# Performance work log

Hardware: AMD Instinct MI355X
Metric: run time of the kernel (lower is better)

The kernel has to match this reference:

```python
import jax, jax.numpy as jnp
import numpy as np

NEG_RATIO = 5          # neg_sample_ratio, also k (num_nodes-1 >> ratio)
THRESH = 0.7           # hard_neg_threshold
SMOOTH = 0.1           # label_smoothing
NUM_NODES = 200_000
DIM = 128
B = 1024               # batch size, all labels == 1 (all positives)
FILL_VAL = -1.0e9


def _l2_normalize(x, eps=1e-12):
    # F.normalize(p=2, dim=-1): divide by clamped L2 norm
    n = jnp.sqrt(jnp.sum(x * x, axis=-1, keepdims=True))
    return x / jnp.maximum(n, eps)


def setup_inputs() -> dict:
    key = jax.random.key(0)
    k1, k2, k3, k4 = jax.random.split(key, 4)
    src_nodes = jax.random.randint(k1, (B,), 0, NUM_NODES)
    dst_nodes = jax.random.randint(k2, (B,), 0, NUM_NODES)
    labels = jnp.ones((B,), dtype=jnp.float32)  # all positives -> pos_mask all True
    timestamps = jax.random.uniform(k3, (B,), dtype=jnp.float32)
    memory = jax.random.normal(k4, (NUM_NODES, DIM), dtype=jnp.float32)
    return {
        "src_nodes": src_nodes,
        "dst_nodes": dst_nodes,
        "labels": labels,
        "timestamps": timestamps,
        "memory": memory,
    }


def reference(src_nodes, dst_nodes, labels, timestamps, memory):
    # --- embedding gather + L2 normalize ---
    src_emb = memory[src_nodes]                      # [B, D]
    s = _l2_normalize(src_emb).astype(jnp.float16)   # use_half_precision=True
    c = _l2_normalize(memory).astype(jnp.float16)    # [N, D]

    # --- similarity [B, N], back to fp32 ---
    sim = jnp.matmul(s, c.T).astype(jnp.float32)

    # --- mask out ground-truth dst and below-threshold sims ---
    cols = jnp.arange(NUM_NODES)
    allowed = cols[None, :] != dst_nodes[:, None]    # exclude GT positives
    valid = allowed & (sim > THRESH)
    score = jnp.where(valid, sim, FILL_VAL)

    # --- top-k hard negatives per positive ---
    k = NEG_RATIO  # min(neg_sample_ratio, num_nodes-1)
    topk_vals, topk_idx = jax.lax.top_k(score, k)    # [B, k]
    is_real = (topk_vals > FILL_VAL + 1.0).reshape(-1)  # [B*k]

    # --- fallback random negatives (fixed-shape equivalent of the torch
    #     pack-real-then-pad-random assembly; total count == B*k either way) ---
    rkey = jax.random.key(42)
    rand_dst = jax.random.randint(rkey, (B * k,), 0, NUM_NODES)
    src_rep = jnp.repeat(src_nodes, k)               # [B*k]
    rand_dst = jnp.where(rand_dst == src_rep, (rand_dst + 1) % NUM_NODES, rand_dst)

    final_src = src_rep
    final_dst = jnp.where(is_real, topk_idx.reshape(-1), rand_dst)
    neg_ts = jnp.repeat(timestamps, k)

    # --- assemble augmented batch ---
    new_src = jnp.concatenate([src_nodes, final_src])
    new_dst = jnp.concatenate([dst_nodes, final_dst])
    new_labels = jnp.concatenate([labels, jnp.zeros((B * k,), labels.dtype)])
    new_ts = jnp.concatenate([timestamps, neg_ts])

    # --- label smoothing ---
    new_labels = new_labels * (1.0 - SMOOTH) + (1.0 - new_labels) * SMOOTH

    return new_src, new_dst, new_labels, new_ts, topk_vals
```

## Files before the change

kernel.cpp:

```cpp
#include <hip/hip_runtime.h>

#define NUM_NODES 200000
#define DIM 128
#define BATCH 1024
#define K_NEG 5
#define CAP 16
#define NBLK 250
#define CPB 800
#define TCOL 32
#define NT 25
#define THRESH 0.7f
#define FILL (-1.0e9f)

typedef __attribute__((ext_vector_type(8))) short short8;
typedef __attribute__((ext_vector_type(16))) float f32x16;

__device__ __forceinline__ unsigned short f2bf(float x) {
  unsigned u = __builtin_bit_cast(unsigned, x);
  return (unsigned short)((u + 0x7fffu + ((u >> 16) & 1u)) >> 16);
}

__device__ __forceinline__ void stage16(const void* g, void* l) {
  __builtin_amdgcn_global_load_lds(
      (const __attribute__((address_space(1))) unsigned int*)g,
      (__attribute__((address_space(3))) unsigned int*)l,
      16, 0, 0);
}

__device__ __forceinline__ void tf2x32(unsigned k0, unsigned k1,
                                       unsigned x0, unsigned x1,
                                       unsigned* o0, unsigned* o1) {
  unsigned ks2 = k0 ^ k1 ^ 0x1BD11BDAu;
  unsigned v0 = x0 + k0, v1 = x1 + k1;
#define TFR(r) { v0 += v1; v1 = (v1 << r) | (v1 >> (32 - r)); v1 ^= v0; }
  TFR(13) TFR(15) TFR(26) TFR(6)   v0 += k1;  v1 += ks2 + 1u;
  TFR(17) TFR(29) TFR(16) TFR(24)  v0 += ks2; v1 += k0 + 2u;
  TFR(13) TFR(15) TFR(26) TFR(6)   v0 += k0;  v1 += k1 + 3u;
  TFR(17) TFR(29) TFR(16) TFR(24)  v0 += k1;  v1 += ks2 + 4u;
  TFR(13) TFR(15) TFR(26) TFR(6)   v0 += ks2; v1 += k0 + 5u;
#undef TFR
  *o0 = v0; *o1 = v1;
}

__device__ __forceinline__ unsigned rbits32(unsigned ka, unsigned kb, unsigned m) {
  unsigned o0, o1;
  tf2x32(ka, kb, 0u, m, &o0, &o1);
  return o0 ^ o1;
}

__global__ void prep_kernel(const float* __restrict__ memory,
                            const int* __restrict__ src_nodes,
                            unsigned short* __restrict__ s16f,
                            int* __restrict__ cand_cnt) {
  int tid = threadIdx.x;
  int gid = blockIdx.x * 256 + tid;
  if (gid < BATCH) cand_cnt[gid] = 0;
  int row = blockIdx.x * 4 + (tid >> 6);
  int L = tid & 63;
  int s = src_nodes[row];
  float2 v = ((const float2*)(memory + (size_t)s * DIM))[L];
  float ss = v.x * v.x + v.y * v.y;
#pragma unroll
  for (int off = 32; off > 0; off >>= 1) ss += __shfl_xor(ss, off);
  float inv = 1.0f / fmaxf(sqrtf(ss), 1e-12f);
  unsigned p = (unsigned)f2bf(v.x * inv) | ((unsigned)f2bf(v.y * inv) << 16);
  int ms = row >> 5, l32 = row & 31;
  int c = L >> 2;
  int ks = c >> 1, half = c & 1;
  ((unsigned*)s16f)[(((ms * 8 + ks) * 64) + half * 32 + l32) * 4 + (L & 3)] = p;
}

__global__ __launch_bounds__(512, 2) void sim_scan_kernel(
    const float* __restrict__ memory,
    const unsigned short* __restrict__ s16f,
    const int* __restrict__ dst_nodes,
    int* __restrict__ cand_cnt,
    float* __restrict__ cand_val,
    int* __restrict__ cand_idx) {
  __shared__ char rawb[16384];
  __shared__ unsigned short fragb[2][4096];
  __shared__ float nrmb[2][32];

  int tid = threadIdx.x;
  int wid = tid >> 6;
  int lane = tid & 63;
  int half = lane >> 5;
  int l32 = lane & 31;
  int jb0 = blockIdx.x * CPB;

  const char* mb = (const char*)memory;

#define STAGE(t) {                                                              \
    int jn = jb0 + (t) * TCOL;                                                  \
    stage16(mb + (size_t)(jn + (tid & 31)) * 512 + ((tid >> 5) << 4),           \
            (char*)rawb + (wid << 10));                                         \
    stage16(mb + (size_t)(jn + (tid & 31)) * 512 + (((tid >> 5) + 16) << 4),    \
            (char*)rawb + 8192 + (wid << 10));                                  \
  }

  int ccol = wid * 4 + (lane & 3);
  int cseg = lane >> 2;
#define CONVERT(p) {                                                            \
    float4 q0 = *(const float4*)(rawb + (((2 * cseg) * 32 + ccol) << 4));       \
    float4 q1 = *(const float4*)(rawb + (((2 * cseg + 1) * 32 + ccol) << 4));   \
    float ss = q0.x * q0.x + q0.y * q0.y + q0.z * q0.z + q0.w * q0.w            \
             + q1.x * q1.x + q1.y * q1.y + q1.z * q1.z + q1.w * q1.w;           \
    ss += __shfl_xor(ss, 4); ss += __shfl_xor(ss, 8);                           \
    ss += __shfl_xor(ss, 16); ss += __shfl_xor(ss, 32);                         \
    short8 f;                                                                   \
    f[0] = (short)f2bf(q0.x); f[1] = (short)f2bf(q0.y);                         \
    f[2] = (short)f2bf(q0.z); f[3] = (short)f2bf(q0.w);                         \
    f[4] = (short)f2bf(q1.x); f[5] = (short)f2bf(q1.y);                         \
    f[6] = (short)f2bf(q1.z); f[7] = (short)f2bf(q1.w);                         \
    *(short8*)((char*)fragb[p] + ((cseg * 32 + ccol) << 4)) = f;                \
    if (cseg == 0) nrmb[p][ccol] = fmaxf(sqrtf(ss), 1e-12f);                    \
  }

  STAGE(0);
  const short8* __restrict__ af = (const short8*)s16f;
  short8 a[4][8];
#pragma unroll
  for (int m = 0; m < 4; ++m)
#pragma unroll
    for (int ks = 0; ks < 8; ++ks)
      a[m][ks] = af[(((wid * 4 + m) * 8) + ks) * 64 + lane];
  __syncthreads();
  CONVERT(0);
  __syncthreads();
  STAGE(1);
  __syncthreads();

  f32x16 Z;
#pragma unroll
  for (int i = 0; i < 16; ++i) Z[i] = 0.0f;

  for (int t = 0; t < NT; ++t) {
    if (t < NT - 1) CONVERT((t + 1) & 1);
    __syncthreads();
    if (t < NT - 2) STAGE(t + 2);

    int p = t & 1;
    float nv = nrmb[p][l32];
    float thr = THRESH * nv;
    float invv = 1.0f / nv;
    int gj = jb0 + t * TCOL + l32;
    short8 bf[8];
#pragma unroll
    for (int ks = 0; ks < 8; ++ks)
      bf[ks] = *(const short8*)((char*)fragb[p] + (((2 * ks + half) * 32 + l32) << 4));

#pragma unroll
    for (int mp = 0; mp < 2; ++mp) {
      f32x16 accA = __builtin_amdgcn_mfma_f32_32x32x16_bf16(a[mp * 2][0], bf[0], Z, 0, 0, 0);
      f32x16 accB = __builtin_amdgcn_mfma_f32_32x32x16_bf16(a[mp * 2 + 1][0], bf[0], Z, 0, 0, 0);
#pragma unroll
      for (int ks = 1; ks < 8; ++ks) {
        accA = __builtin_amdgcn_mfma_f32_32x32x16_bf16(a[mp * 2][ks], bf[ks], accA, 0, 0, 0);
        accB = __builtin_amdgcn_mfma_f32_32x32x16_bf16(a[mp * 2 + 1][ks], bf[ks], accB, 0, 0, 0);
      }
      float mA = accA[0], mB = accB[0];
#pragma unroll
      for (int i = 1; i < 16; ++i) { mA = fmaxf(mA, accA[i]); mB = fmaxf(mB, accB[i]); }
      if (mA > thr || mB > thr) {
#pragma unroll
        for (int e = 0; e < 2; ++e) {
#pragma unroll
          for (int r = 0; r < 16; ++r) {
            float raw = (e == 0) ? accA[r] : accB[r];
            if (raw > thr) {
              int gi = (wid * 4 + mp * 2 + e) * 32 + (r & 3) + 8 * (r >> 2) + 4 * half;
              if (gj != dst_nodes[gi]) {
                int pq = atomicAdd(&cand_cnt[gi], 1);
                if (pq < CAP) {
                  cand_val[gi * CAP + pq] = raw * invv;
                  cand_idx[gi * CAP + pq] = gj;
                }
              }
            }
          }
        }
      }
    }

    __syncthreads();
  }
#undef STAGE
#undef CONVERT
}

__global__ void finalize_kernel(const int* __restrict__ src_nodes,
                                const int* __restrict__ dst_nodes,
                                const float* __restrict__ labels,
                                const float* __restrict__ ts,
                                const int* __restrict__ cand_cnt,
                                const float* __restrict__ cand_val,
                                const int* __restrict__ cand_idx,
                                float* __restrict__ out) {
  int r = blockIdx.x * 256 + threadIdx.x;
  if (r >= BATCH) return;
  const int TOT = BATCH + BATCH * K_NEG;
  int srcv = src_nodes[r];
  float tsv = ts[r];
  out[r] = (float)srcv;
  out[TOT + r] = (float)dst_nodes[r];
  float l = labels[r];
  out[2 * TOT + r] = l * 0.9f + (1.0f - l) * 0.1f;
  out[3 * TOT + r] = tsv;

  int cnt = cand_cnt[r];
  cnt = cnt < CAP ? cnt : CAP;
  float cv[CAP]; int ci[CAP];
  for (int i = 0; i < cnt; ++i) { cv[i] = cand_val[r * CAP + i]; ci[i] = cand_idx[r * CAP + i]; }

  unsigned k1a, k1b, k2a, k2b;
  tf2x32(0u, 42u, 0u, 0u, &k1a, &k1b);
  tf2x32(0u, 42u, 0u, 1u, &k2a, &k2b);

  const unsigned span = 200000u;
  const unsigned mult = 167296u;

  for (int s = 0; s < K_NEG; ++s) {
    int sel = -1;
    for (int i = 0; i < cnt; ++i)
      if (sel < 0 || cv[i] > cv[sel] || (cv[i] == cv[sel] && ci[i] < ci[sel])) sel = i;
    float v = FILL; int idx = 0;
    if (sel >= 0) { v = cv[sel]; idx = ci[sel]; cv[sel] = FILL; ci[sel] = 0x7fffffff; }
    bool is_real = v > (FILL + 1.0f);

    unsigned m = (unsigned)(r * K_NEG + s);
    unsigned hi = rbits32(k1a, k1b, m);
    unsigned lo = rbits32(k2a, k2b, m);
    unsigned off = ((hi % span) * mult + (lo % span)) % span;
    int rd = (int)off;
    if (rd == srcv) rd = (rd + 1) % NUM_NODES;
    int fd = is_real ? idx : rd;

    int mi = (int)m;
    out[BATCH + mi] = (float)srcv;
    out[TOT + BATCH + mi] = (float)fd;
    out[2 * TOT + BATCH + mi] = 0.1f;
    out[3 * TOT + BATCH + mi] = tsv;
    out[4 * TOT + mi] = v;
  }
}

extern "C" void kernel_launch(void* const* d_in, const int* in_sizes, int n_in,
                              void* d_out, int out_size, void* d_ws, size_t ws_size,
                              hipStream_t stream) {
  const int* src = (const int*)d_in[0];
  const int* dst = (const int*)d_in[1];
  const float* labels = (const float*)d_in[2];
  const float* ts = (const float*)d_in[3];
  const float* memory = (const float*)d_in[4];
  float* out = (float*)d_out;

  char* ws = (char*)d_ws;
  unsigned short* s16f = (unsigned short*)ws;
  int* cand_cnt = (int*)(ws + 262144);
  float* cand_val = (float*)(ws + 266240);
  int* cand_idx = (int*)(ws + 331776);

  prep_kernel<<<256, 256, 0, stream>>>(memory, src, s16f, cand_cnt);
  sim_scan_kernel<<<NBLK, 512, 0, stream>>>(memory, s16f, dst, cand_cnt, cand_val, cand_idx);
  finalize_kernel<<<(BATCH + 255) / 256, 256, 0, stream>>>(src, dst, labels, ts,
                                                           cand_cnt, cand_val, cand_idx, out);
}
```

Before: 188.5 us.

## Double-buffer raw LDS staging with XOR swizzle and drop a barrier

```diff
diff --git a/kernel.cpp b/kernel.cpp
--- a/kernel.cpp
+++ b/kernel.cpp
@@ -77,7 +77,7 @@
     int* __restrict__ cand_cnt,
     float* __restrict__ cand_val,
     int* __restrict__ cand_idx) {
-  __shared__ char rawb[16384];
+  __shared__ char rawb[2][16384];
   __shared__ unsigned short fragb[2][4096];
   __shared__ float nrmb[2][32];
 
@@ -90,19 +90,25 @@
 
   const char* mb = (const char*)memory;
 
-#define STAGE(t) {                                                              \
+#define STAGE(t, rbuf) {                                                        \
     int jn = jb0 + (t) * TCOL;                                                  \
-    stage16(mb + (size_t)(jn + (tid & 31)) * 512 + ((tid >> 5) << 4),           \
-            (char*)rawb + (wid << 10));                                         \
-    stage16(mb + (size_t)(jn + (tid & 31)) * 512 + (((tid >> 5) + 16) << 4),    \
-            (char*)rawb + 8192 + (wid << 10));                                  \
+    int u1 = tid;                                                               \
+    int g1 = (u1 & 31) ^ ((u1 >> 6) & 7);                                       \
+    stage16(mb + (size_t)(jn + g1) * 512 + ((u1 >> 5) << 4),                    \
+            (char*)(rbuf) + (wid << 10));                                       \
+    int u2 = tid + 512;                                                         \
+    int g2 = (u2 & 31) ^ ((u2 >> 6) & 7);                                       \
+    stage16(mb + (size_t)(jn + g2) * 512 + ((u2 >> 5) << 4),                    \
+            (char*)(rbuf) + 8192 + (wid << 10));                                \
   }
 
   int ccol = wid * 4 + (lane & 3);
   int cseg = lane >> 2;
-#define CONVERT(p) {                                                            \
-    float4 q0 = *(const float4*)(rawb + (((2 * cseg) * 32 + ccol) << 4));       \
-    float4 q1 = *(const float4*)(rawb + (((2 * cseg + 1) * 32 + ccol) << 4));   \
+#define CONVERT(p, rbuf) {                                                      \
+    const char* rb = (const char*)(rbuf);                                       \
+    int xc = ccol ^ (cseg & 7);                                                 \
+    float4 q0 = *(const float4*)(rb + (((2 * cseg) * 32 + xc) << 4));           \
+    float4 q1 = *(const float4*)(rb + (((2 * cseg + 1) * 32 + xc) << 4));       \
     float ss = q0.x * q0.x + q0.y * q0.y + q0.z * q0.z + q0.w * q0.w            \
              + q1.x * q1.x + q1.y * q1.y + q1.z * q1.z + q1.w * q1.w;           \
     ss += __shfl_xor(ss, 4); ss += __shfl_xor(ss, 8);                           \
@@ -116,7 +122,7 @@
     if (cseg == 0) nrmb[p][ccol] = fmaxf(sqrtf(ss), 1e-12f);                    \
   }
 
-  STAGE(0);
+  STAGE(0, rawb[0]);
   const short8* __restrict__ af = (const short8*)s16f;
   short8 a[4][8];
 #pragma unroll
@@ -125,29 +131,27 @@
     for (int ks = 0; ks < 8; ++ks)
       a[m][ks] = af[(((wid * 4 + m) * 8) + ks) * 64 + lane];
   __syncthreads();
-  CONVERT(0);
+  CONVERT(0, rawb[0]);
+  STAGE(1, rawb[1]);
   __syncthreads();
-  STAGE(1);
-  __syncthreads();
 
   f32x16 Z;
 #pragma unroll
   for (int i = 0; i < 16; ++i) Z[i] = 0.0f;
 
   for (int t = 0; t < NT; ++t) {
-    if (t < NT - 1) CONVERT((t + 1) & 1);
-    __syncthreads();
-    if (t < NT - 2) STAGE(t + 2);
-
-    int p = t & 1;
-    float nv = nrmb[p][l32];
+    int par = t & 1;
+    if (t + 2 < NT) STAGE(t + 2, rawb[par]);
+    if (t + 1 < NT) CONVERT(par ^ 1, rawb[par ^ 1]);
+
+    float nv = nrmb[par][l32];
     float thr = THRESH * nv;
     float invv = 1.0f / nv;
     int gj = jb0 + t * TCOL + l32;
     short8 bf[8];
 #pragma unroll
     for (int ks = 0; ks < 8; ++ks)
-      bf[ks] = *(const short8*)((char*)fragb[p] + (((2 * ks + half) * 32 + l32) << 4));
+      bf[ks] = *(const short8*)((char*)fragb[par] + (((2 * ks + half) * 32 + l32) << 4));
 
 #pragma unroll
     for (int mp = 0; mp < 2; ++mp) {
```

Result: slower. 206.0 us (+9.3%).
